# Performance work log

Measured on AMD Instinct MI355X. Metric: run time of the kernel, lower is better.

The kernel has to match this reference:

```python
import jax, jax.numpy as jnp
import numpy as np

K = 1.0  # Lorentz curvature
N, H, IN_S, OUT_S = 4096, 12, 256, 128  # nodes, heads, spatial in/out dims


def _midpoint_norm(ave):
    # Lorentz midpoint normalization: sqrt(K) * ave / sqrt(|<ave,ave>_L|)
    inner = -ave[..., 0:1] ** 2 + jnp.sum(ave[..., 1:] ** 2, axis=-1, keepdims=True)
    denom = jnp.sqrt(jnp.maximum(jnp.abs(inner), 1e-8))
    return jnp.sqrt(K) * ave / denom


def setup_inputs() -> dict:
    key = jax.random.key(0)
    ks = jax.random.split(key, 8)
    xs = jax.random.normal(ks[0], (N, IN_S), jnp.float32)
    xt = jnp.sqrt(jnp.sum(xs * xs, axis=-1, keepdims=True) + K)
    x_lorentz = jnp.concatenate([xt, xs], axis=-1)  # [N, 257] on the manifold
    std = 1.0 / np.sqrt(IN_S)
    def lin(k1, k2):
        W = jax.random.uniform(k1, (H, OUT_S, IN_S), jnp.float32, -std, std)
        b = jax.random.uniform(k2, (H, OUT_S), jnp.float32, -std, std)
        return W, b
    Wq, bq = lin(ks[1], ks[2])
    Wk, bk = lin(ks[3], ks[4])
    Wv, bv = lin(ks[5], ks[6])
    scale = jnp.array([np.sqrt(OUT_S + 1)], jnp.float32)  # sqrt(out_channels)
    bias = jnp.zeros((), jnp.float32)
    return {"x_lorentz": x_lorentz, "Wq": Wq, "bq": bq, "Wk": Wk, "bk": bk,
            "Wv": Wv, "bv": bv, "scale": scale, "bias": bias}


def reference(x_lorentz, Wq, bq, Wk, bk, Wv, bv, scale, bias):
    xs = x_lorentz[..., 1:]  # drop time coord: [N, IN_S]

    def hyp_linear(W, b):
        # per-head linear on spatial part, then reconstruct Lorentz time coord
        s = jnp.einsum('ni,hoi->hno', xs, W) + b[:, None, :]  # [H, N, OUT_S]
        t = jnp.sqrt(jnp.sum(s * s, axis=-1, keepdims=True) + K)
        return jnp.concatenate([t, s], axis=-1)  # [H, N, OUT_S+1]

    q = hyp_linear(Wq, bq)
    k = hyp_linear(Wk, bk)
    v = hyp_linear(Wv, bv)

    # Lorentz inner product scores: <q,k>_L = -q0*k0 + q_s . k_s
    sgn = jnp.concatenate([-jnp.ones((1,), q.dtype), jnp.ones((q.shape[-1] - 1,), q.dtype)])
    att = 2.0 + 2.0 * jnp.einsum('hnd,hmd->hnm', q * sgn, k)  # [H, N, N]
    att = att / scale + bias
    att = jax.nn.softmax(att, axis=-1)

    # weighted Lorentz midpoint per head
    ave = jnp.einsum('hnm,hmd->hnd', att, v)
    out = _midpoint_norm(ave)           # [H, N, D]
    out = out.transpose(1, 0, 2)        # [N, H, D]
    # uniform midpoint across heads
    out = _midpoint_norm(out.mean(axis=-2))  # [N, D]
    return out
```

## Files before the change

### kernel.cpp

```cpp
#include <hip/hip_runtime.h>
#include <hip/hip_bf16.h>

#define NT   4096
#define NH   12
#define INS  256
#define DOUT 128
#define D1   129

typedef short bf16x8  __attribute__((ext_vector_type(8)));
typedef float f32x4   __attribute__((ext_vector_type(4)));
typedef float f32x16  __attribute__((ext_vector_type(16)));

__device__ __forceinline__ short f2bf(float f) {
  union { __hip_bfloat16 h; short s; } u;
  u.h = __float2bfloat16(f);
  return u.s;
}

#define MFMA16(a,b,c) __builtin_amdgcn_mfma_f32_16x16x32_bf16((a),(b),(c),0,0,0)
#define MFMA32(a,b,c) __builtin_amdgcn_mfma_f32_32x32x16_bf16((a),(b),(c),0,0,0)

#define GL2LDS(gp, lp) \
  __builtin_amdgcn_global_load_lds((const __attribute__((address_space(1))) unsigned*)(gp), \
                                   (__attribute__((address_space(3))) unsigned*)(lp), 16, 0, 0)


__global__ void k_cvt_xs(const float* __restrict__ xl, short* __restrict__ xs) {
  int i = blockIdx.x * 256 + threadIdx.x;
  int row = i >> 8, col = i & 255;
  xs[i] = f2bf(xl[row * 257 + 1 + col]);
}

__global__ void k_cvt_w(const float* __restrict__ w0, const float* __restrict__ w1,
                        const float* __restrict__ w2, short* __restrict__ dst) {
  int i = blockIdx.x * 256 + threadIdx.x;
  const float* s = blockIdx.y == 0 ? w0 : (blockIdx.y == 1 ? w1 : w2);
  dst[(size_t)blockIdx.y * (NH * DOUT * INS) + i] = f2bf(s[i]);
}


__launch_bounds__(256, 2)
__global__ void k_proj(const short* __restrict__ xs, const short* __restrict__ Wb,
                       const float* __restrict__ b0, const float* __restrict__ b1,
                       const float* __restrict__ b2, const float* __restrict__ scalep,
                       short* __restrict__ Qb, short* __restrict__ Kb, short* __restrict__ VT,
                       float* __restrict__ qt, float* __restrict__ ktP, float* __restrict__ vtP) {
  __shared__ __align__(16) short lds_t[128 * 144];
  int t = threadIdx.x, l = t & 63, w = t >> 6;
  int lr = l & 15, lg = l >> 4;
  int h = blockIdx.y, z = blockIdx.z;
  int n0w = blockIdx.x * 128 + w * 32;
  const short* Wh = Wb + ((size_t)z * NH + h) * DOUT * INS;
  const float* bias = z == 0 ? b0 : (z == 1 ? b1 : b2);

  f32x4 acc[2][8] = {};
#pragma unroll
  for (int dk = 0; dk < 8; ++dk) {
    bf16x8 a[2], b[8];
#pragma unroll
    for (int qf = 0; qf < 2; ++qf)
      a[qf] = *(const bf16x8*)(xs + (size_t)(n0w + 16 * qf + lr) * INS + dk * 32 + lg * 8);
#pragma unroll
    for (int cf = 0; cf < 8; ++cf)
      b[cf] = *(const bf16x8*)(Wh + (size_t)(lr + 16 * cf) * INS + dk * 32 + lg * 8);
#pragma unroll
    for (int qf = 0; qf < 2; ++qf)
#pragma unroll
      for (int cf = 0; cf < 8; ++cf)
        acc[qf][cf] = MFMA16(a[qf], b[cf], acc[qf][cf]);
  }

  float tval[2][4];
#pragma unroll
  for (int qf = 0; qf < 2; ++qf) {
    float ssq[4] = {0.f, 0.f, 0.f, 0.f};
#pragma unroll
    for (int cf = 0; cf < 8; ++cf) {
      float bv = bias[h * DOUT + lr + 16 * cf];
#pragma unroll
      for (int r = 0; r < 4; ++r) {
        acc[qf][cf][r] += bv;
        ssq[r] += acc[qf][cf][r] * acc[qf][cf][r];
      }
    }
#pragma unroll
    for (int r = 0; r < 4; ++r) {
      float s = ssq[r];
      s += __shfl_xor(s, 1); s += __shfl_xor(s, 2);
      s += __shfl_xor(s, 4); s += __shfl_xor(s, 8);
      tval[qf][r] = sqrtf(s + 1.0f);
    }
  }

  float c2 = 2.0f * 1.442695040888963f / scalep[0];

  if (z < 2) {
    float f = (z == 0) ? c2 : 1.0f;
#pragma unroll
    for (int qf = 0; qf < 2; ++qf)
#pragma unroll
      for (int cf = 0; cf < 8; ++cf)
#pragma unroll
        for (int r = 0; r < 4; ++r)
          lds_t[(w * 32 + 16 * qf + lg * 4 + r) * 136 + lr + 16 * cf] = f2bf(acc[qf][cf][r] * f);
    if (lr == 0) {
#pragma unroll
      for (int qf = 0; qf < 2; ++qf)
#pragma unroll
        for (int r = 0; r < 4; ++r) {
          int n = n0w + 16 * qf + lg * 4 + r;
          if (z == 0) {
            qt[(size_t)h * NT + n] = tval[qf][r] * f;
          } else {
            int ml = n & 31, g = n >> 5;
            int hh = (ml >> 2) & 1, j = (ml & 3) + 4 * (ml >> 3);
            ktP[(size_t)h * NT + g * 32 + hh * 16 + j] = tval[qf][r];
          }
        }
    }
    __syncthreads();
    int row = t >> 1, half = t & 1;
    const short* src = lds_t + row * 136 + half * 64;
    short* dst = (z == 0 ? Qb : Kb) + ((size_t)h * NT + blockIdx.x * 128 + row) * DOUT + half * 64;
#pragma unroll
    for (int j = 0; j < 8; ++j)
      *(bf16x8*)(dst + j * 8) = *(const bf16x8*)(src + j * 8);
  } else {
#pragma unroll
    for (int qf = 0; qf < 2; ++qf)
#pragma unroll
      for (int cf = 0; cf < 8; ++cf)
#pragma unroll
        for (int r = 0; r < 4; ++r)
          lds_t[(lr + 16 * cf) * 144 + w * 32 + 16 * qf + lg * 4 + r] = f2bf(acc[qf][cf][r]);
    if (lr == 0) {
#pragma unroll
      for (int qf = 0; qf < 2; ++qf)
#pragma unroll
        for (int r = 0; r < 4; ++r) {
          int n = n0w + 16 * qf + lg * 4 + r;
          int ml = n & 31, g = n >> 5;
          int hh = (ml >> 2) & 1, j = (ml & 3) + 4 * (ml >> 3);
          vtP[(size_t)h * NT + g * 32 + hh * 16 + j] = tval[qf][r];
        }
    }
    __syncthreads();
    int d = t >> 1, half = t & 1;
    const short* src = lds_t + d * 144 + half * 64;
    short* dst = VT + ((size_t)h * DOUT + d) * NT + blockIdx.x * 128 + half * 64;
#pragma unroll
    for (int j = 0; j < 8; ++j)
      *(bf16x8*)(dst + j * 8) = *(const bf16x8*)(src + j * 8);
  }
}


template <int NZ, int ATOMIC>
__launch_bounds__(256, 3)
__global__ void k_attn(const short* __restrict__ Qb, const short* __restrict__ Kb,
                       const short* __restrict__ VT,
                       const float* __restrict__ qt, const float* __restrict__ ktP,
                       const float* __restrict__ vtP,
                       float* __restrict__ partz, float* __restrict__ avtz) {
  __shared__ __align__(16) char lds_all[32768];
  char* lds_k = lds_all;
  char* lds_v = lds_all + 16384;

  int t = threadIdx.x, l = t & 63, w = t >> 6;
  int ql = l & 31, hi = l >> 5;

  int bid = blockIdx.x;
  int xcd = bid & 7, j = bid >> 3;
  int x = j & 31;
  int g = xcd + 8 * (j >> 5);
  int h = g % NH, z = g / NH;

  constexpr int KPERZ = NT / (NZ * 64);
  int n0w = x * 128 + w * 32;
  int n = n0w + ql;

  const short* Qh = Qb + (size_t)h * NT * DOUT;
  const short* Kh = Kb + (size_t)h * NT * DOUT;
  const short* VTh = VT + (size_t)h * DOUT * NT;
  const float* ktPh = ktP + (size_t)h * NT;
  const float* vtPh = vtP + (size_t)h * NT;

  bf16x8 bq[8];
#pragma unroll
  for (int dk = 0; dk < 8; ++dk)
    bq[dk] = *(const bf16x8*)(Qh + (size_t)n * DOUT + dk * 16 + hi * 8);
  float qc2 = qt[(size_t)h * NT + n];

  f32x16 accO[4] = {};
  float avt = 0.f;

  int mz = z * (NT / NZ);

#pragma unroll
  for (int it = 0; it < 4; ++it) {
    int c = t + it * 256;
    int m = c >> 4, s = c & 15;
    GL2LDS(Kh + (size_t)(mz + m) * DOUT + ((s ^ (m & 15)) * 8), lds_k + c * 16);
  }

  for (int ktile = 0; ktile < KPERZ; ++ktile) {
    int m0 = mz + ktile * 64;
    __syncthreads();

#pragma unroll
    for (int it = 0; it < 4; ++it) {
      int c = t + it * 256;
      int d = c >> 3, s = c & 7;
      GL2LDS(VTh + (size_t)d * NT + m0 + ((s ^ (d & 7)) * 8), lds_v + c * 16);
    }

    bf16x8 pfrag[4];
#pragma unroll
    for (int mf = 0; mf < 2; ++mf) {
      f32x16 accS = {};
      int m = mf * 32 + ql;
      int rowb = m * 256;
      int sx = m & 15;
      __builtin_amdgcn_s_setprio(1);
#pragma unroll
      for (int dk = 0; dk < 8; ++dk) {
        bf16x8 ak = *(const bf16x8*)(lds_k + rowb + (((dk * 2 + hi) ^ sx) * 16));
        accS = MFMA32(ak, bq[dk], accS);
      }
      __builtin_amdgcn_s_setprio(0);

      const float* ktm = ktPh + m0 + mf * 32 + hi * 16;
      const float* vtm = vtPh + m0 + mf * 32 + hi * 16;
      unsigned pk[8];
#pragma unroll
      for (int i4 = 0; i4 < 4; ++i4) {
        f32x4 kt4 = *(const f32x4*)(ktm + i4 * 4);
        f32x4 vt4 = *(const f32x4*)(vtm + i4 * 4);
#pragma unroll
        for (int ii = 0; ii < 2; ++ii) {
          float a0 = fmaf(-qc2, kt4[2 * ii],     accS[i4 * 4 + 2 * ii]);
          float a1 = fmaf(-qc2, kt4[2 * ii + 1], accS[i4 * 4 + 2 * ii + 1]);
          float p0, p1;
          asm("v_exp_f32 %0, %1" : "=v"(p0) : "v"(a0));
          asm("v_exp_f32 %0, %1" : "=v"(p1) : "v"(a1));
          avt = fmaf(p0, vt4[2 * ii], avt);
          avt = fmaf(p1, vt4[2 * ii + 1], avt);
          unsigned pw;
          asm("v_cvt_pk_bf16_f32 %0, %1, %2" : "=v"(pw) : "v"(p0), "v"(p1));
          pk[i4 * 2 + ii] = pw;
        }
      }
      asm volatile("v_permlane32_swap_b32 %0, %1" : "+v"(pk[0]), "+v"(pk[2]));
      asm volatile("v_permlane32_swap_b32 %0, %1" : "+v"(pk[1]), "+v"(pk[3]));
      asm volatile("v_permlane32_swap_b32 %0, %1" : "+v"(pk[4]), "+v"(pk[6]));
      asm volatile("v_permlane32_swap_b32 %0, %1" : "+v"(pk[5]), "+v"(pk[7]));
      union { unsigned u[4]; bf16x8 v; } f0, f1;
      f0.u[0] = pk[0]; f0.u[1] = pk[1]; f0.u[2] = pk[2]; f0.u[3] = pk[3];
      f1.u[0] = pk[4]; f1.u[1] = pk[5]; f1.u[2] = pk[6]; f1.u[3] = pk[7];
      pfrag[2 * mf] = f0.v;
      pfrag[2 * mf + 1] = f1.v;
    }

    __syncthreads();

    if (ktile + 1 < KPERZ) {
      int m1 = m0 + 64;
#pragma unroll
      for (int it = 0; it < 4; ++it) {
        int c = t + it * 256;
        int m = c >> 4, s = c & 15;
        GL2LDS(Kh + (size_t)(m1 + m) * DOUT + ((s ^ (m & 15)) * 8), lds_k + c * 16);
      }
    }

    __builtin_amdgcn_s_setprio(1);
#pragma unroll
    for (int ks = 0; ks < 4; ++ks) {
#pragma unroll
      for (int df = 0; df < 4; ++df) {
        int d = df * 32 + ql;
        bf16x8 av = *(const bf16x8*)(lds_v + d * 128 + (((ks * 2 + hi) ^ (d & 7)) * 16));
        accO[df] = MFMA32(av, pfrag[ks], accO[df]);
      }
    }
    __builtin_amdgcn_s_setprio(0);
  }

  __syncthreads();
  float* sc = (float*)(lds_all + w * 8192);
  int zb = ATOMIC ? 0 : z;
  float* wbase = partz + (((size_t)zb * NH + h) * NT + n0w) * 128;
#pragma unroll
  for (int dh = 0; dh < 2; ++dh) {
#pragma unroll
    for (int j2 = 0; j2 < 2; ++j2)
#pragma unroll
      for (int r = 0; r < 16; ++r) {
        int dl = j2 * 32 + (r & 3) + 8 * (r >> 2) + 4 * hi;
        sc[ql * 64 + (dl ^ ql)] = accO[2 * dh + j2][r];
      }
    __syncthreads();
#pragma unroll
    for (int nl = 0; nl < 32; ++nl) {
      float v = sc[nl * 64 + (l ^ nl)];
      if (ATOMIC) atomicAdd(wbase + (size_t)nl * 128 + dh * 64 + l, v);
      else        wbase[(size_t)nl * 128 + dh * 64 + l] = v;
    }
    __syncthreads();
  }
  float avt2 = avt + __shfl_xor(avt, 32);
  if (l < 32) {
    float* ap = avtz + ((size_t)zb * NH + h) * NT + n0w + ql;
    if (ATOMIC) atomicAdd(ap, avt2);
    else        *ap = avt2;
  }
}


__global__ void k_comb(const float* __restrict__ partz, const float* __restrict__ avtz,
                       float* __restrict__ out, int nbuf) {
  int l = threadIdx.x & 63, w = threadIdx.x >> 6;
  int n = blockIdx.x * 4 + w;
  float acc_lo = 0.f, acc_hi = 0.f, acc_t = 0.f;
#pragma unroll
  for (int h = 0; h < NH; ++h) {
    float x = 0.f, y = 0.f, at = 0.f;
    for (int zb = 0; zb < nbuf; ++zb) {
      const float* p = partz + (((size_t)zb * NH + h) * NT + n) * 128;
      x += p[l]; y += p[64 + l];
      at += avtz[((size_t)zb * NH + h) * NT + n];
    }
    float sp = x * x + y * y;
    sp += __shfl_xor(sp, 1);  sp += __shfl_xor(sp, 2);
    sp += __shfl_xor(sp, 4);  sp += __shfl_xor(sp, 8);
    sp += __shfl_xor(sp, 16); sp += __shfl_xor(sp, 32);
    float inner = sp - at * at;
    float rd = 1.0f / sqrtf(fmaxf(fabsf(inner), 1e-8f));
    acc_lo += x * rd; acc_hi += y * rd; acc_t += at * rd;
  }
  float sp = acc_lo * acc_lo + acc_hi * acc_hi;
  sp += __shfl_xor(sp, 1);  sp += __shfl_xor(sp, 2);
  sp += __shfl_xor(sp, 4);  sp += __shfl_xor(sp, 8);
  sp += __shfl_xor(sp, 16); sp += __shfl_xor(sp, 32);
  float inner = sp - acc_t * acc_t;
  float rd = 1.0f / sqrtf(fmaxf(fabsf(inner), 1e-8f));
  float* orow = out + (size_t)n * D1;
  orow[1 + l] = acc_lo * rd;
  orow[65 + l] = acc_hi * rd;
  if (l == 0) orow[0] = acc_t * rd;
}


extern "C" void kernel_launch(void* const* d_in, const int* in_sizes, int n_in,
                              void* d_out, int out_size, void* d_ws, size_t ws_size,
                              hipStream_t stream) {
  (void)in_sizes; (void)n_in; (void)out_size;
  const float* xl    = (const float*)d_in[0];
  const float* Wq    = (const float*)d_in[1];
  const float* bq    = (const float*)d_in[2];
  const float* Wk    = (const float*)d_in[3];
  const float* bk    = (const float*)d_in[4];
  const float* Wv    = (const float*)d_in[5];
  const float* bv    = (const float*)d_in[6];
  const float* scale = (const float*)d_in[7];
  float* out = (float*)d_out;

  char* ws = (char*)d_ws;
  size_t off = 0;
  auto alloc = [&](size_t b) { char* p = ws + off; off = (off + b + 255) & ~(size_t)255; return p; };
  auto al = [](size_t b) { return (b + 255) & ~(size_t)255; };

  short* Qb    = (short*)alloc((size_t)NH * NT * DOUT * 2);
  short* Kb    = (short*)alloc((size_t)NH * NT * DOUT * 2);
  short* VT    = (short*)alloc((size_t)NH * DOUT * NT * 2);
  float* qt    = (float*)alloc((size_t)NH * NT * 4);
  float* ktP   = (float*)alloc((size_t)NH * NT * 4);
  float* vtP   = (float*)alloc((size_t)NH * NT * 4);
  size_t base = off;

  size_t xs_b = al((size_t)NT * INS * 2);
  size_t wb_b = al((size_t)3 * NH * DOUT * INS * 2);
  size_t projtmp = xs_b + wb_b;
  auto part_b = [&](int nb) {
    return al((size_t)nb * NH * NT * 128 * 4) + al((size_t)nb * NH * NT * 4);
  };

  int nbuf, atomic;
  if (ws_size >= base + (projtmp > part_b(2) ? projtmp : part_b(2))) {
    nbuf = 2; atomic = 0;
  } else {
    nbuf = 1; atomic = 1;
  }

  char* region = ws + base;
  short* xs    = (short*)region;
  short* Wb    = (short*)(region + xs_b);
  float* partz = (float*)region;
  float* avtz  = (float*)(region + al((size_t)nbuf * NH * NT * 128 * 4));

  if (atomic)
    hipMemsetAsync(partz, 0, part_b(1), stream);

  k_cvt_xs<<<NT, 256, 0, stream>>>(xl, xs);
  k_cvt_w<<<dim3(NH * DOUT * INS / 256, 3), 256, 0, stream>>>(Wq, Wk, Wv, Wb);
  k_proj<<<dim3(NT / 128, NH, 3), 256, 0, stream>>>(xs, Wb, bq, bk, bv, scale, Qb, Kb, VT, qt, ktP, vtP);
  if (atomic)
    k_attn<2, 1><<<(NT / 128) * NH * 2, 256, 0, stream>>>(Qb, Kb, VT, qt, ktP, vtP, partz, avtz);
  else
    k_attn<2, 0><<<(NT / 128) * NH * 2, 256, 0, stream>>>(Qb, Kb, VT, qt, ktP, vtP, partz, avtz);
  k_comb<<<NT / 4, 256, 0, stream>>>(partz, avtz, out, nbuf);
}
```

Baseline: 293.0 us.

## Double-buffer V tiles in LDS, load K directly to registers, fuse conversion kernels

```diff
diff --git a/kernel.cpp b/kernel.cpp
--- a/kernel.cpp
+++ b/kernel.cpp
@@ -25,17 +25,31 @@
                                    (__attribute__((address_space(3))) unsigned*)(lp), 16, 0, 0)
 
 
-__global__ void k_cvt_xs(const float* __restrict__ xl, short* __restrict__ xs) {
-  int i = blockIdx.x * 256 + threadIdx.x;
-  int row = i >> 8, col = i & 255;
-  xs[i] = f2bf(xl[row * 257 + 1 + col]);
-}
-
-__global__ void k_cvt_w(const float* __restrict__ w0, const float* __restrict__ w1,
-                        const float* __restrict__ w2, short* __restrict__ dst) {
-  int i = blockIdx.x * 256 + threadIdx.x;
-  const float* s = blockIdx.y == 0 ? w0 : (blockIdx.y == 1 ? w1 : w2);
-  dst[(size_t)blockIdx.y * (NH * DOUT * INS) + i] = f2bf(s[i]);
+__global__ void k_cvt(const float* __restrict__ xl,
+                      const float* __restrict__ w0, const float* __restrict__ w1,
+                      const float* __restrict__ w2,
+                      short* __restrict__ xs, short* __restrict__ Wb) {
+  int b = blockIdx.x, t = threadIdx.x;
+  if (b < 1024) {
+    int i = b * 256 + t;
+#pragma unroll
+    for (int p = 0; p < 4; ++p, i += 262144) {
+      int row = i >> 8, col = i & 255;
+      xs[i] = f2bf(xl[row * 257 + 1 + col]);
+    }
+  } else {
+    const int M = NH * DOUT * INS;
+    int i = ((b - 1024) * 256 + t) * 8;
+    int zz = i / M;
+    int rem = i - zz * M;
+    const float* s = (zz == 0 ? w0 : (zz == 1 ? w1 : w2)) + rem;
+    float4 a = *(const float4*)(s);
+    float4 c = *(const float4*)(s + 4);
+    union { short sh[8]; bf16x8 v; } o;
+    o.sh[0] = f2bf(a.x); o.sh[1] = f2bf(a.y); o.sh[2] = f2bf(a.z); o.sh[3] = f2bf(a.w);
+    o.sh[4] = f2bf(c.x); o.sh[5] = f2bf(c.y); o.sh[6] = f2bf(c.z); o.sh[7] = f2bf(c.w);
+    *(bf16x8*)(Wb + i) = o.v;
+  }
 }
 
 
@@ -163,8 +177,6 @@
                        const float* __restrict__ vtP,
                        float* __restrict__ partz, float* __restrict__ avtz) {
   __shared__ __align__(16) char lds_all[32768];
-  char* lds_k = lds_all;
-  char* lds_v = lds_all + 16384;
 
   int t = threadIdx.x, l = t & 63, w = t >> 6;
   int ql = l & 31, hi = l >> 5;
@@ -196,37 +208,43 @@
 
   int mz = z * (NT / NZ);
 
+  int vc = t;
+
 #pragma unroll
   for (int it = 0; it < 4; ++it) {
-    int c = t + it * 256;
-    int m = c >> 4, s = c & 15;
-    GL2LDS(Kh + (size_t)(mz + m) * DOUT + ((s ^ (m & 15)) * 8), lds_k + c * 16);
+    int c = vc + it * 256;
+    int d = c >> 3, s = c & 7;
+    GL2LDS(VTh + (size_t)d * NT + mz + ((s ^ (d & 7)) * 8), lds_all + c * 16);
   }
 
   for (int ktile = 0; ktile < KPERZ; ++ktile) {
     int m0 = mz + ktile * 64;
+    char* vcur = lds_all + (ktile & 1) * 16384;
     __syncthreads();
 
-#pragma unroll
-    for (int it = 0; it < 4; ++it) {
-      int c = t + it * 256;
-      int d = c >> 3, s = c & 7;
-      GL2LDS(VTh + (size_t)d * NT + m0 + ((s ^ (d & 7)) * 8), lds_v + c * 16);
-    }
-
-    bf16x8 pfrag[4];
+    if (ktile + 1 < KPERZ) {
+      char* vnxt = lds_all + ((ktile + 1) & 1) * 16384;
+      int m1 = m0 + 64;
+#pragma unroll
+      for (int it = 0; it < 4; ++it) {
+        int c = vc + it * 256;
+        int d = c >> 3, s = c & 7;
+        GL2LDS(VTh + (size_t)d * NT + m1 + ((s ^ (d & 7)) * 8), vnxt + c * 16);
+      }
+    }
+
 #pragma unroll
     for (int mf = 0; mf < 2; ++mf) {
+      const short* Kp = Kh + (size_t)(m0 + mf * 32 + ql) * DOUT + hi * 8;
+      bf16x8 ak[8];
+#pragma unroll
+      for (int dk = 0; dk < 8; ++dk)
+        ak[dk] = *(const bf16x8*)(Kp + dk * 16);
       f32x16 accS = {};
-      int m = mf * 32 + ql;
-      int rowb = m * 256;
-      int sx = m & 15;
       __builtin_amdgcn_s_setprio(1);
 #pragma unroll
-      for (int dk = 0; dk < 8; ++dk) {
-        bf16x8 ak = *(const bf16x8*)(lds_k + rowb + (((dk * 2 + hi) ^ sx) * 16));
-        accS = MFMA32(ak, bq[dk], accS);
-      }
+      for (int dk = 0; dk < 8; ++dk)
+        accS = MFMA32(ak[dk], bq[dk], accS);
       __builtin_amdgcn_s_setprio(0);
 
       const float* ktm = ktPh + m0 + mf * 32 + hi * 16;
@@ -257,33 +275,21 @@
       union { unsigned u[4]; bf16x8 v; } f0, f1;
       f0.u[0] = pk[0]; f0.u[1] = pk[1]; f0.u[2] = pk[2]; f0.u[3] = pk[3];
       f1.u[0] = pk[4]; f1.u[1] = pk[5]; f1.u[2] = pk[6]; f1.u[3] = pk[7];
-      pfrag[2 * mf] = f0.v;
-      pfrag[2 * mf + 1] = f1.v;
-    }
-
-    __syncthreads();
-
-    if (ktile + 1 < KPERZ) {
-      int m1 = m0 + 64;
-#pragma unroll
-      for (int it = 0; it < 4; ++it) {
-        int c = t + it * 256;
-        int m = c >> 4, s = c & 15;
-        GL2LDS(Kh + (size_t)(m1 + m) * DOUT + ((s ^ (m & 15)) * 8), lds_k + c * 16);
+
+      __builtin_amdgcn_s_setprio(1);
+#pragma unroll
+      for (int kss = 0; kss < 2; ++kss) {
+        int ks = 2 * mf + kss;
+        bf16x8 pf = kss ? f1.v : f0.v;
+#pragma unroll
+        for (int df = 0; df < 4; ++df) {
+          int d = df * 32 + ql;
+          bf16x8 av = *(const bf16x8*)(vcur + d * 128 + (((ks * 2 + hi) ^ (d & 7)) * 16));
+          accO[df] = MFMA32(av, pf, accO[df]);
+        }
       }
-    }
-
-    __builtin_amdgcn_s_setprio(1);
-#pragma unroll
-    for (int ks = 0; ks < 4; ++ks) {
-#pragma unroll
-      for (int df = 0; df < 4; ++df) {
-        int d = df * 32 + ql;
-        bf16x8 av = *(const bf16x8*)(lds_v + d * 128 + (((ks * 2 + hi) ^ (d & 7)) * 16));
-        accO[df] = MFMA32(av, pfrag[ks], accO[df]);
-      }
-    }
-    __builtin_amdgcn_s_setprio(0);
+      __builtin_amdgcn_s_setprio(0);
+    }
   }
 
   __syncthreads();
@@ -401,8 +407,7 @@
   if (atomic)
     hipMemsetAsync(partz, 0, part_b(1), stream);
 
-  k_cvt_xs<<<NT, 256, 0, stream>>>(xl, xs);
-  k_cvt_w<<<dim3(NH * DOUT * INS / 256, 3), 256, 0, stream>>>(Wq, Wk, Wv, Wb);
+  k_cvt<<<1600, 256, 0, stream>>>(xl, Wq, Wk, Wv, xs, Wb);
   k_proj<<<dim3(NT / 128, NH, 3), 256, 0, stream>>>(xs, Wb, bq, bk, bv, scale, Qb, Kb, VT, qt, ktP, vtP);
   if (atomic)
     k_attn<2, 1><<<(NT / 128) * NH * 2, 256, 0, stream>>>(Qb, Kb, VT, qt, ktP, vtP, partz, avtz);
```

Result: slower. 423.6 us (+44.6%).
